# Performance work log

Hardware: AMD Instinct MI355X
Metric: run time of the kernel (lower is better)

The kernel has to match this reference:

```python
import jax, jax.numpy as jnp
import numpy as np

E = 192; Q = 48; H = 3; HD = Q // H  # per-branch embed 48, 3 heads of 16
CONV_CH = 4; K = 15; PAD = K // 2


def layer_norm(x, g, b, eps=1e-6):
    m = jnp.mean(x, axis=-1, keepdims=True)
    v = jnp.mean((x - m) ** 2, axis=-1, keepdims=True)
    return (x - m) * jax.lax.rsqrt(v + eps) * g + b


def mha(x, w_in, b_in, w_o, b_o):
    # x: [B,S,48]; torch nn.MultiheadAttention math (dropout=eval/identity)
    B, S, _ = x.shape
    qkv = x @ w_in.T + b_in                      # [B,S,144]
    q, k, v = jnp.split(qkv, 3, axis=-1)
    q = q.reshape(B, S, H, HD)
    k = k.reshape(B, S, H, HD)
    v = v.reshape(B, S, H, HD)
    scores = jnp.einsum('bqhd,bkhd->bhqk', q, k) / jnp.sqrt(jnp.float32(HD))
    attn = jax.nn.softmax(scores, axis=-1)
    out = jnp.einsum('bhqk,bkhd->bqhd', attn, v).reshape(B, S, Q)
    return out @ w_o.T + b_o


def light_conv(x96, conv_w):
    # x96: [B,S,96] -> view(-1, 4, 96), depthwise conv1d (k=15, pad=7), view back
    B, S, W = x96.shape
    r = x96.reshape(-1, CONV_CH, W)              # [B*S/... wait: B*S*96/(4*96)=B*S/4? No: reshape(-1,4,96) => [B*S, ...]
    y = jax.lax.conv_general_dilated(
        r, conv_w, window_strides=(1,), padding=[(PAD, PAD)],
        dimension_numbers=('NCH', 'OIH', 'NCH'), feature_group_count=CONV_CH)
    return y.reshape(B, S, W)


def setup_inputs() -> dict:
    key = jax.random.key(0)
    ks = jax.random.split(key, 16)
    sc = 0.05
    d = {
        'x': jax.random.normal(ks[0], (128, 512, E), dtype=jnp.float32),
        'ln1_g': jnp.ones((E,), jnp.float32), 'ln1_b': jnp.zeros((E,), jnp.float32),
        'acc_wqkv': jax.random.normal(ks[1], (3 * Q, Q), jnp.float32) * sc,
        'acc_bqkv': jnp.zeros((3 * Q,), jnp.float32),
        'acc_wo': jax.random.normal(ks[2], (Q, Q), jnp.float32) * sc,
        'acc_bo': jnp.zeros((Q,), jnp.float32),
        'gyro_wqkv': jax.random.normal(ks[3], (3 * Q, Q), jnp.float32) * sc,
        'gyro_bqkv': jnp.zeros((3 * Q,), jnp.float32),
        'gyro_wo': jax.random.normal(ks[4], (Q, Q), jnp.float32) * sc,
        'gyro_bo': jnp.zeros((Q,), jnp.float32),
        'conv_w': jax.random.normal(ks[5], (CONV_CH, 1, K), jnp.float32) * sc,
        'ln2_g': jnp.ones((E,), jnp.float32), 'ln2_b': jnp.zeros((E,), jnp.float32),
        'w1': jax.random.normal(ks[6], (2 * E, E), jnp.float32) * sc,
        'b1': jnp.zeros((2 * E,), jnp.float32),
        'w2': jax.random.normal(ks[7], (E, 2 * E), jnp.float32) * sc,
        'b2': jnp.zeros((E,), jnp.float32),
    }
    return d


def reference(x, ln1_g, ln1_b, acc_wqkv, acc_bqkv, acc_wo, acc_bo,
              gyro_wqkv, gyro_bqkv, gyro_wo, gyro_bo, conv_w,
              ln2_g, ln2_b, w1, b1, w2, b2):
    xn = layer_norm(x, ln1_g, ln1_b)
    x_conv = light_conv(xn[:, :, 48:144], conv_w)
    x_acc = mha(xn[:, :, 0:48], acc_wqkv, acc_bqkv, acc_wo, acc_bo)
    x_gyro = mha(xn[:, :, 96:144], gyro_wqkv, gyro_bqkv, gyro_wo, gyro_bo)
    xcat = jnp.concatenate([x_acc, x_conv, x_gyro], axis=2)
    x1 = xcat + x
    tt = layer_norm(x1, ln2_g, ln2_b)
    tt = jax.nn.relu(tt @ w1.T + b1)
    tt = jax.nn.relu(tt @ w2.T + b2)
    return x1 + tt
```

## Files before the change

kernel.cpp:

```cpp
#include <hip/hip_runtime.h>
#include <stdint.h>

typedef unsigned short u16;
typedef short bf16x8 __attribute__((ext_vector_type(8)));
typedef float f32x4 __attribute__((ext_vector_type(4)));
typedef float f32x16 __attribute__((ext_vector_type(16)));
typedef uint32_t u32x4 __attribute__((ext_vector_type(4)));

#define NB   128
#define SEQ  512
#define EMB  192
#define NTOK (NB * SEQ)
#define F1DIM 384
#define ATTW 192
#define VTP  520
#define KTS  24
#define XnS  200
#define H1S  392

__device__ __forceinline__ float bf2f(u16 u) {
  union { uint32_t u; float f; } v; v.u = ((uint32_t)u) << 16; return v.f;
}
__device__ __forceinline__ u16 f2bf(float f) {
  union { float f; uint32_t u; } v; v.f = f;
  uint32_t r = v.u + 0x7fffu + ((v.u >> 16) & 1u);
  return (u16)(r >> 16);
}
__device__ __forceinline__ uint32_t pack2bf(float a, float b) {
  return (uint32_t)f2bf(a) | ((uint32_t)f2bf(b) << 16);
}

__global__ __launch_bounds__(256) void pack_kernel(const float* __restrict__ w1,
    const float* __restrict__ w2, const float* __restrict__ wqa,
    const float* __restrict__ wqg, const float* __restrict__ woa,
    const float* __restrict__ wog, u16* __restrict__ w1b, u16* __restrict__ w2b,
    u16* __restrict__ wqp, u16* __restrict__ wop) {
  int idx = (int)blockIdx.x * 256 + (int)threadIdx.x;
  if (idx < 73728) {
    w1b[idx] = f2bf(w1[idx]);
  } else if (idx < 147456) {
    w2b[idx - 73728] = f2bf(w2[idx - 73728]);
  } else if (idx < 165888) {
    int i = idx - 147456;
    int row = i >> 6, k = i & 63;
    float v = 0.0f;
    if (k < 48) v = (row < 144) ? wqa[row * 48 + k] : wqg[(row - 144) * 48 + k];
    wqp[i] = f2bf(v);
  } else if (idx < 172032) {
    int i = idx - 165888;
    int row = i >> 6, k = i & 63;
    float v = 0.0f;
    if (k < 48) v = (row < 48) ? woa[row * 48 + k] : wog[(row - 48) * 48 + k];
    wop[i] = f2bf(v);
  }
}

__global__ __launch_bounds__(256) void ln1_qkv_conv_kernel(
    const float* __restrict__ x, const float* __restrict__ g,
    const float* __restrict__ b, const u16* __restrict__ wq,
    const float* __restrict__ bacc, const float* __restrict__ bgyr,
    const float* __restrict__ cw, u16* __restrict__ qkv,
    u16* __restrict__ att) {
  __shared__ u16 Xn[64 * XnS];
  int bm = (int)blockIdx.x * 64;
  int tid = threadIdx.x;
  int trow = tid >> 2, part = tid & 3;
  int tok = bm + trow;
  const float* xr = x + (size_t)tok * EMB + part * 48;
  float vals[48];
#pragma unroll
  for (int j = 0; j < 48; j += 4) {
    float4 v = *(const float4*)(xr + j);
    vals[j] = v.x; vals[j + 1] = v.y; vals[j + 2] = v.z; vals[j + 3] = v.w;
  }
  float s = 0.0f, s2 = 0.0f;
#pragma unroll
  for (int j = 0; j < 48; j++) { s += vals[j]; s2 += vals[j] * vals[j]; }
  s += __shfl_xor(s, 1); s2 += __shfl_xor(s2, 1);
  s += __shfl_xor(s, 2); s2 += __shfl_xor(s2, 2);
  float mean = s * (1.0f / EMB);
  float var  = s2 * (1.0f / EMB) - mean * mean;
  float rs   = rsqrtf(var + 1e-6f);
  {
    u16* xnrow = Xn + trow * XnS + part * 48;
    const float* gp = g + part * 48;
    const float* bp = b + part * 48;
#pragma unroll
    for (int j = 0; j < 48; j += 2) {
      uint32_t w = pack2bf((vals[j] - mean) * rs * gp[j] + bp[j],
                           (vals[j + 1] - mean) * rs * gp[j + 1] + bp[j + 1]);
      *(uint32_t*)(xnrow + j) = w;
    }
  }
  __syncthreads();
  int wid = tid >> 6, lane = tid & 63;
  int l15 = lane & 15, quad = lane >> 4;
  const u16* arow_l = Xn + (wid * 16 + l15) * XnS;
  f32x4 acc[18] = {};
#pragma unroll
  for (int ks = 0; ks < 2; ks++) {
    int kk = ks * 32;
    bf16x8 af_a = *(const bf16x8*)(arow_l + kk + quad * 8);
    bf16x8 af_g = *(const bf16x8*)(arow_l + 96 + kk + quad * 8);
#pragma unroll
    for (int st = 0; st < 18; st++) {
      bf16x8 bf = *(const bf16x8*)(wq + (size_t)(st * 16 + l15) * 64 + kk + quad * 8);
      acc[st] = __builtin_amdgcn_mfma_f32_16x16x32_bf16(st < 9 ? af_a : af_g,
                                                        bf, acc[st], 0, 0, 0);
    }
  }
#pragma unroll
  for (int st = 0; st < 18; st++) {
    int col = st * 16 + l15;
    int cc = (col < 144) ? col : col - 144;
    float bias = (col < 144) ? bacc[cc] : bgyr[cc];
    float qs = (cc < 48) ? 0.36067376022f : 1.0f;
#pragma unroll
    for (int r = 0; r < 4; r++) {
      int orow = bm + wid * 16 + quad * 4 + r;
      qkv[(size_t)orow * 288 + col] = f2bf((acc[st][r] + bias) * qs);
    }
  }
  {
    int wr = trow & 3;
    float w15[15];
#pragma unroll
    for (int k = 0; k < 15; k++) w15[k] = cw[wr * 15 + k];
    float win[38];
    int base = part * 24 - 7;
#pragma unroll
    for (int i = 0; i < 38; i++) {
      int p = base + i;
      win[i] = (p >= 0 && p < 96) ? bf2f(Xn[trow * XnS + 48 + p]) : 0.0f;
    }
    const float* xres = x + (size_t)tok * EMB + 48 + part * 24;
    u16* orow = att + (size_t)tok * ATTW + 96 + part * 24;
#pragma unroll
    for (int c = 0; c < 24; c += 4) {
      float4 r4 = *(const float4*)(xres + c);
      float o[4];
#pragma unroll
      for (int u = 0; u < 4; u++) {
        float sc = 0.0f;
#pragma unroll
        for (int k = 0; k < 15; k++) sc += win[c + u + k] * w15[k];
        o[u] = sc;
      }
      *(uint32_t*)(orow + c)     = pack2bf(o[0] + r4.x, o[1] + r4.y);
      *(uint32_t*)(orow + c + 2) = pack2bf(o[2] + r4.z, o[3] + r4.w);
    }
  }
}

__global__ __launch_bounds__(256) void attn_kernel(const u16* __restrict__ qkv,
                                                   u16* __restrict__ att) {
  __shared__ u16 Kt[SEQ * KTS];
  __shared__ u16 Vt[17 * VTP];
  int bid = blockIdx.x;
  int hh  = bid % 3;
  int brb = (bid / 3) & 1;
  int b   = bid / 6;
  int tid = threadIdx.x;
  size_t tokbase = (size_t)b * SEQ;
  int qoff = brb * 144 + hh * 16;
  int koff = qoff + 48;
  int voff = qoff + 96;
  for (int r = tid; r < SEQ; r += 256) {
    const u16* src = qkv + (tokbase + r) * 288;
    *(uint4*)(Kt + r * KTS)     = *(const uint4*)(src + koff);
    *(uint4*)(Kt + r * KTS + 8) = *(const uint4*)(src + koff + 8);
    u16 tmp[16];
    *(uint4*)(tmp)     = *(const uint4*)(src + voff);
    *(uint4*)(tmp + 8) = *(const uint4*)(src + voff + 8);
#pragma unroll
    for (int j = 0; j < 16; j++) Vt[j * VTP + r] = tmp[j];
  }
  Vt[16 * VTP + tid]       = 0x3F80;
  Vt[16 * VTP + 256 + tid] = 0x3F80;
  __syncthreads();
  int wave = tid >> 6, lane = tid & 63;
  int q31 = lane & 31, h = lane >> 5;
  int dcl = (q31 < 16) ? q31 : 16;
#pragma unroll 1
  for (int qi = 0; qi < 4; qi++) {
    int qrow = (wave * 4 + qi) * 32 + q31;
    bf16x8 qfrag = *(const bf16x8*)(qkv + (tokbase + qrow) * 288 + qoff + h * 8);
    f32x16 Ot = {};
#pragma unroll 2
    for (int kt = 0; kt < 16; kt++) {
      bf16x8 kfrag = *(const bf16x8*)(Kt + (kt * 32 + q31) * KTS + h * 8);
      f32x16 zc = {};
      f32x16 S = __builtin_amdgcn_mfma_f32_32x32x16_bf16(kfrag, qfrag, zc, 0, 0, 0);
      uint32_t pk[8], swk[8];
#pragma unroll
      for (int i = 0; i < 8; i++) {
        union { float f; uint32_t u; } a0, a1;
        a0.f = exp2f(S[2 * i]);
        a1.f = exp2f(S[2 * i + 1]);
        pk[i] = __builtin_amdgcn_perm(a1.u, a0.u, 0x07060302u);
        swk[i] = (uint32_t)__shfl_xor((int)pk[i], 32);
      }
      u32x4 t1 = { h ? swk[2] : pk[0], h ? swk[3] : pk[1],
                   h ? pk[2]  : swk[0], h ? pk[3]  : swk[1] };
      u32x4 t2 = { h ? swk[6] : pk[4], h ? swk[7] : pk[5],
                   h ? pk[6]  : swk[4], h ? pk[7]  : swk[5] };
      bf16x8 pb1 = __builtin_bit_cast(bf16x8, t1);
      bf16x8 pb2 = __builtin_bit_cast(bf16x8, t2);
      bf16x8 av1 = *(const bf16x8*)(Vt + dcl * VTP + kt * 32 + h * 8);
      bf16x8 av2 = *(const bf16x8*)(Vt + dcl * VTP + kt * 32 + 16 + h * 8);
      Ot = __builtin_amdgcn_mfma_f32_32x32x16_bf16(av1, pb1, Ot, 0, 0, 0);
      Ot = __builtin_amdgcn_mfma_f32_32x32x16_bf16(av2, pb2, Ot, 0, 0, 0);
    }
    float inv = 1.0f / Ot[8];
    u16* orow = att + (tokbase + qrow) * ATTW + brb * 48 + hh * 16 + 4 * h;
    uint2 st0 = { pack2bf(Ot[0] * inv, Ot[1] * inv),
                  pack2bf(Ot[2] * inv, Ot[3] * inv) };
    uint2 st1 = { pack2bf(Ot[4] * inv, Ot[5] * inv),
                  pack2bf(Ot[6] * inv, Ot[7] * inv) };
    *(uint2*)(orow)     = st0;
    *(uint2*)(orow + 8) = st1;
  }
}

__global__ __launch_bounds__(256) void tail_kernel(
    const u16* __restrict__ att, const u16* __restrict__ wo,
    const float* __restrict__ boacc, const float* __restrict__ bogyr,
    const float* __restrict__ x, const float* __restrict__ g2,
    const float* __restrict__ b2v, const u16* __restrict__ w1b,
    const float* __restrict__ b1, const u16* __restrict__ w2b,
    const float* __restrict__ b2, float* __restrict__ out) {
  __shared__ u16 LDSB[32 * XnS + 32 * H1S];
  u16* X1b = LDSB;
  u16* Tn  = LDSB + 32 * XnS;
  u16* H1  = LDSB + 32 * XnS;
  int bm = (int)blockIdx.x * 32;
  int tid = threadIdx.x;
  int wid = tid >> 6, lane = tid & 63;
  int l15 = lane & 15, quad = lane >> 4;
  {
    int trow = tid >> 3, p8 = tid & 7;
    const u16* src = att + (size_t)(bm + trow) * ATTW + 96 + p8 * 12;
    u16* dst = X1b + trow * XnS + 48 + p8 * 12;
    *(uint2*)(dst)     = *(const uint2*)(src);
    *(uint2*)(dst + 4) = *(const uint2*)(src + 4);
    *(uint2*)(dst + 8) = *(const uint2*)(src + 8);
  }
  {
    int mt = wid & 1, ng = wid >> 1;
    int row = bm + mt * 16 + l15;
    const u16* arow = att + (size_t)row * ATTW + (ng ? 48 : 0);
    f32x4 acc[3] = {};
#pragma unroll
    for (int ks = 0; ks < 2; ks++) {
      int kk = ks * 32;
      bf16x8 af = *(const bf16x8*)(arow + kk + quad * 8);
#pragma unroll
      for (int st = 0; st < 3; st++) {
        int stg = ng * 3 + st;
        bf16x8 bf = *(const bf16x8*)(wo + (size_t)(stg * 16 + l15) * 64 + kk + quad * 8);
        acc[st] = __builtin_amdgcn_mfma_f32_16x16x32_bf16(af, bf, acc[st], 0, 0, 0);
      }
    }
#pragma unroll
    for (int st = 0; st < 3; st++) {
      int col = (ng * 3 + st) * 16 + l15;
      float bias = (col < 48) ? boacc[col] : bogyr[col - 48];
      int oc = (col < 48) ? col : col + 96;
#pragma unroll
      for (int r = 0; r < 4; r++) {
        int lrow = mt * 16 + quad * 4 + r;
        float v = acc[st][r] + bias + x[(size_t)(bm + lrow) * EMB + oc];
        X1b[lrow * XnS + oc] = f2bf(v);
      }
    }
  }
  __syncthreads();
  {
    int trow = tid >> 3, part = tid & 7;
    const u16* xl = X1b + trow * XnS + part * 24;
    float vals[24];
    {
      u16 raw[24];
      *(uint4*)(raw)      = *(const uint4*)(xl);
      *(uint4*)(raw + 8)  = *(const uint4*)(xl + 8);
      *(uint4*)(raw + 16) = *(const uint4*)(xl + 16);
#pragma unroll
      for (int j = 0; j < 24; j++) vals[j] = bf2f(raw[j]);
    }
    float s = 0.0f, s2 = 0.0f;
#pragma unroll
    for (int j = 0; j < 24; j++) { s += vals[j]; s2 += vals[j] * vals[j]; }
    s += __shfl_xor(s, 1); s2 += __shfl_xor(s2, 1);
    s += __shfl_xor(s, 2); s2 += __shfl_xor(s2, 2);
    s += __shfl_xor(s, 4); s2 += __shfl_xor(s2, 4);
    float mean = s * (1.0f / EMB);
    float var  = s2 * (1.0f / EMB) - mean * mean;
    float rs   = rsqrtf(var + 1e-6f);
    u16* trp = Tn + trow * XnS + part * 24;
    const float* gp = g2 + part * 24;
    const float* bp = b2v + part * 24;
#pragma unroll
    for (int j = 0; j < 24; j += 2) {
      uint32_t w = pack2bf((vals[j] - mean) * rs * gp[j] + bp[j],
                           (vals[j + 1] - mean) * rs * gp[j + 1] + bp[j + 1]);
      *(uint32_t*)(trp + j) = w;
    }
  }
  __syncthreads();
  int ng1 = wid;
  f32x4 acc1[12] = {};
#pragma unroll
  for (int kk = 0; kk < 192; kk += 32) {
    bf16x8 a0 = *(const bf16x8*)(Tn + (l15) * XnS + kk + quad * 8);
    bf16x8 a1 = *(const bf16x8*)(Tn + (16 + l15) * XnS + kk + quad * 8);
#pragma unroll
    for (int stl = 0; stl < 6; stl++) {
      bf16x8 bf = *(const bf16x8*)(w1b + (size_t)((ng1 * 6 + stl) * 16 + l15) * EMB + kk + quad * 8);
      acc1[stl]     = __builtin_amdgcn_mfma_f32_16x16x32_bf16(a0, bf, acc1[stl], 0, 0, 0);
      acc1[6 + stl] = __builtin_amdgcn_mfma_f32_16x16x32_bf16(a1, bf, acc1[6 + stl], 0, 0, 0);
    }
  }
  __syncthreads();
#pragma unroll
  for (int stl = 0; stl < 6; stl++) {
    int col = (ng1 * 6 + stl) * 16 + l15;
    float bias = b1[col];
#pragma unroll
    for (int m2 = 0; m2 < 2; m2++) {
#pragma unroll
      for (int r = 0; r < 4; r++) {
        float v = acc1[m2 * 6 + stl][r] + bias;
        v = v > 0.0f ? v : 0.0f;
        H1[(m2 * 16 + quad * 4 + r) * H1S + col] = f2bf(v);
      }
    }
  }
  __syncthreads();
  {
    int ng2 = wid;
    f32x4 acc2[6] = {};
#pragma unroll
    for (int kk = 0; kk < 384; kk += 32) {
      bf16x8 a0 = *(const bf16x8*)(H1 + (l15) * H1S + kk + quad * 8);
      bf16x8 a1 = *(const bf16x8*)(H1 + (16 + l15) * H1S + kk + quad * 8);
#pragma unroll
      for (int stl = 0; stl < 3; stl++) {
        bf16x8 bf = *(const bf16x8*)(w2b + (size_t)((ng2 * 3 + stl) * 16 + l15) * F1DIM + kk + quad * 8);
        acc2[stl]     = __builtin_amdgcn_mfma_f32_16x16x32_bf16(a0, bf, acc2[stl], 0, 0, 0);
        acc2[3 + stl] = __builtin_amdgcn_mfma_f32_16x16x32_bf16(a1, bf, acc2[3 + stl], 0, 0, 0);
      }
    }
#pragma unroll
    for (int stl = 0; stl < 3; stl++) {
      int col = (ng2 * 3 + stl) * 16 + l15;
      float bias = b2[col];
#pragma unroll
      for (int m2 = 0; m2 < 2; m2++) {
#pragma unroll
        for (int r = 0; r < 4; r++) {
          int lrow = m2 * 16 + quad * 4 + r;
          float v = acc2[m2 * 3 + stl][r] + bias;
          v = v > 0.0f ? v : 0.0f;
          out[(size_t)(bm + lrow) * EMB + col] = v + bf2f(X1b[lrow * XnS + col]);
        }
      }
    }
  }
}

extern "C" void kernel_launch(void* const* d_in, const int* in_sizes, int n_in,
                              void* d_out, int out_size, void* d_ws, size_t ws_size,
                              hipStream_t stream) {
  const float* x         = (const float*)d_in[0];
  const float* ln1_g     = (const float*)d_in[1];
  const float* ln1_b     = (const float*)d_in[2];
  const float* acc_wqkv  = (const float*)d_in[3];
  const float* acc_bqkv  = (const float*)d_in[4];
  const float* acc_wo    = (const float*)d_in[5];
  const float* acc_bo    = (const float*)d_in[6];
  const float* gyro_wqkv = (const float*)d_in[7];
  const float* gyro_bqkv = (const float*)d_in[8];
  const float* gyro_wo   = (const float*)d_in[9];
  const float* gyro_bo   = (const float*)d_in[10];
  const float* conv_w    = (const float*)d_in[11];
  const float* ln2_g     = (const float*)d_in[12];
  const float* ln2_b     = (const float*)d_in[13];
  const float* w1        = (const float*)d_in[14];
  const float* b1        = (const float*)d_in[15];
  const float* w2        = (const float*)d_in[16];
  const float* b2        = (const float*)d_in[17];
  float* out = (float*)d_out;
  char* ws = (char*)d_ws;

  u16* qkvb = (u16*)(ws);
  u16* attb = (u16*)(ws + 37748736);
  u16* w1b  = (u16*)(ws + 62914560);
  u16* w2b  = (u16*)(ws + 63062016);
  u16* wqp  = (u16*)(ws + 63209472);
  u16* wop  = (u16*)(ws + 63246336);

  pack_kernel<<<672, 256, 0, stream>>>(w1, w2, acc_wqkv, gyro_wqkv, acc_wo,
                                       gyro_wo, w1b, w2b, wqp, wop);
  ln1_qkv_conv_kernel<<<NTOK / 64, 256, 0, stream>>>(
      x, ln1_g, ln1_b, wqp, acc_bqkv, gyro_bqkv, conv_w, qkvb, attb);
  attn_kernel<<<NB * 6, 256, 0, stream>>>(qkvb, attb);
  tail_kernel<<<NTOK / 32, 256, 0, stream>>>(
      attb, wop, acc_bo, gyro_bo, x, ln2_g, ln2_b, w1b, b1, w2b, b2, out);
}
```

Baseline: 317.6 us.

## Halve tail kernel row tile to 16 and prefetch first MLP weight fragments

The tail kernel now processes 16 tokens per block instead of 32, which halves the accumulator registers and LDS per block and doubles the grid, with a launch bound asking for 6 blocks per CU. The first k-slice of the W1 and W2 fragments is loaded into registers at kernel start so those loads overlap the out-projection and layernorm phases. The out-projection work is redistributed: three waves do the MFMAs and one wave copies the conv columns. In exchange, each weight fragment is reused across only one 16-row tile, so global/L2 weight traffic per token doubles.

Result: slower. 395.4 us (+24.5%).

```diff
diff --git a/kernel.cpp b/kernel.cpp
--- a/kernel.cpp
+++ b/kernel.cpp
@@ -222,147 +222,161 @@
   }
 }
 
-__global__ __launch_bounds__(256) void tail_kernel(
+__global__ __launch_bounds__(256, 6) void tail_kernel(
     const u16* __restrict__ att, const u16* __restrict__ wo,
     const float* __restrict__ boacc, const float* __restrict__ bogyr,
     const float* __restrict__ x, const float* __restrict__ g2,
     const float* __restrict__ b2v, const u16* __restrict__ w1b,
     const float* __restrict__ b1, const u16* __restrict__ w2b,
     const float* __restrict__ b2, float* __restrict__ out) {
-  __shared__ u16 LDSB[32 * XnS + 32 * H1S];
+  __shared__ u16 LDSB[32 * XnS + 16 * H1S];
   u16* X1b = LDSB;
-  u16* Tn  = LDSB + 32 * XnS;
+  u16* Tn  = LDSB + 16 * XnS;
   u16* H1  = LDSB + 32 * XnS;
-  int bm = (int)blockIdx.x * 32;
+  int bm = (int)blockIdx.x * 16;
   int tid = threadIdx.x;
   int wid = tid >> 6, lane = tid & 63;
   int l15 = lane & 15, quad = lane >> 4;
-  {
-    int trow = tid >> 3, p8 = tid & 7;
-    const u16* src = att + (size_t)(bm + trow) * ATTW + 96 + p8 * 12;
-    u16* dst = X1b + trow * XnS + 48 + p8 * 12;
-    *(uint2*)(dst)     = *(const uint2*)(src);
-    *(uint2*)(dst + 4) = *(const uint2*)(src + 4);
-    *(uint2*)(dst + 8) = *(const uint2*)(src + 8);
-  }
-  {
-    int mt = wid & 1, ng = wid >> 1;
-    int row = bm + mt * 16 + l15;
-    const u16* arow = att + (size_t)row * ATTW + (ng ? 48 : 0);
-    f32x4 acc[3] = {};
+
+  bf16x8 pw1[6], pw2[3];
+#pragma unroll
+  for (int stl = 0; stl < 6; stl++)
+    pw1[stl] = *(const bf16x8*)(w1b + (size_t)((wid * 6 + stl) * 16 + l15) * EMB + quad * 8);
+#pragma unroll
+  for (int stl = 0; stl < 3; stl++)
+    pw2[stl] = *(const bf16x8*)(w2b + (size_t)((wid * 3 + stl) * 16 + l15) * F1DIM + quad * 8);
+
+  if (wid == 3) {
+    int trow = lane >> 2, p4 = lane & 3;
+    const u16* src = att + (size_t)(bm + trow) * ATTW + 96 + p4 * 24;
+    u16* dst = X1b + trow * XnS + 48 + p4 * 24;
+    *(uint4*)(dst)      = *(const uint4*)(src);
+    *(uint4*)(dst + 8)  = *(const uint4*)(src + 8);
+    *(uint4*)(dst + 16) = *(const uint4*)(src + 16);
+  } else {
+    const u16* arow0 = att + (size_t)(bm + l15) * ATTW;
+    bf16x8 afA[2], afG[2];
 #pragma unroll
     for (int ks = 0; ks < 2; ks++) {
-      int kk = ks * 32;
-      bf16x8 af = *(const bf16x8*)(arow + kk + quad * 8);
-#pragma unroll
-      for (int st = 0; st < 3; st++) {
-        int stg = ng * 3 + st;
-        bf16x8 bf = *(const bf16x8*)(wo + (size_t)(stg * 16 + l15) * 64 + kk + quad * 8);
-        acc[st] = __builtin_amdgcn_mfma_f32_16x16x32_bf16(af, bf, acc[st], 0, 0, 0);
-      }
-    }
-#pragma unroll
-    for (int st = 0; st < 3; st++) {
-      int col = (ng * 3 + st) * 16 + l15;
+      afA[ks] = *(const bf16x8*)(arow0 + ks * 32 + quad * 8);
+      afG[ks] = *(const bf16x8*)(arow0 + 48 + ks * 32 + quad * 8);
+    }
+    f32x4 acc[2] = {};
+#pragma unroll
+    for (int s = 0; s < 2; s++) {
+      int st = wid * 2 + s;
+      int ng = (st >= 3) ? 1 : 0;
+#pragma unroll
+      for (int ks = 0; ks < 2; ks++) {
+        bf16x8 bf = *(const bf16x8*)(wo + (size_t)(st * 16 + l15) * 64 + ks * 32 + quad * 8);
+        acc[s] = __builtin_amdgcn_mfma_f32_16x16x32_bf16(ng ? afG[ks] : afA[ks],
+                                                         bf, acc[s], 0, 0, 0);
+      }
+    }
+#pragma unroll
+    for (int s = 0; s < 2; s++) {
+      int st = wid * 2 + s;
+      int col = st * 16 + l15;
       float bias = (col < 48) ? boacc[col] : bogyr[col - 48];
       int oc = (col < 48) ? col : col + 96;
 #pragma unroll
       for (int r = 0; r < 4; r++) {
-        int lrow = mt * 16 + quad * 4 + r;
-        float v = acc[st][r] + bias + x[(size_t)(bm + lrow) * EMB + oc];
+        int lrow = quad * 4 + r;
+        float v = acc[s][r] + bias + x[(size_t)(bm + lrow) * EMB + oc];
         X1b[lrow * XnS + oc] = f2bf(v);
       }
     }
   }
   __syncthreads();
+
   {
-    int trow = tid >> 3, part = tid & 7;
-    const u16* xl = X1b + trow * XnS + part * 24;
-    float vals[24];
-    {
-      u16 raw[24];
-      *(uint4*)(raw)      = *(const uint4*)(xl);
-      *(uint4*)(raw + 8)  = *(const uint4*)(xl + 8);
-      *(uint4*)(raw + 16) = *(const uint4*)(xl + 16);
-#pragma unroll
-      for (int j = 0; j < 24; j++) vals[j] = bf2f(raw[j]);
-    }
+    int trow = tid >> 4, part = tid & 15;
+    const u16* xl = X1b + trow * XnS + part * 12;
+    u16 raw[12];
+    *(uint2*)(raw)     = *(const uint2*)(xl);
+    *(uint2*)(raw + 4) = *(const uint2*)(xl + 4);
+    *(uint2*)(raw + 8) = *(const uint2*)(xl + 8);
+    float vals[12];
+#pragma unroll
+    for (int j = 0; j < 12; j++) vals[j] = bf2f(raw[j]);
     float s = 0.0f, s2 = 0.0f;
 #pragma unroll
-    for (int j = 0; j < 24; j++) { s += vals[j]; s2 += vals[j] * vals[j]; }
+    for (int j = 0; j < 12; j++) { s += vals[j]; s2 += vals[j] * vals[j]; }
     s += __shfl_xor(s, 1); s2 += __shfl_xor(s2, 1);
     s += __shfl_xor(s, 2); s2 += __shfl_xor(s2, 2);
     s += __shfl_xor(s, 4); s2 += __shfl_xor(s2, 4);
+    s += __shfl_xor(s, 8); s2 += __shfl_xor(s2, 8);
     float mean = s * (1.0f / EMB);
     float var  = s2 * (1.0f / EMB) - mean * mean;
     float rs   = rsqrtf(var + 1e-6f);
-    u16* trp = Tn + trow * XnS + part * 24;
-    const float* gp = g2 + part * 24;
-    const float* bp = b2v + part * 24;
-#pragma unroll
-    for (int j = 0; j < 24; j += 2) {
+    u16* trp = Tn + trow * XnS + part * 12;
+    const float* gp = g2 + part * 12;
+    const float* bp = b2v + part * 12;
+#pragma unroll
+    for (int j = 0; j < 12; j += 2) {
       uint32_t w = pack2bf((vals[j] - mean) * rs * gp[j] + bp[j],
                            (vals[j + 1] - mean) * rs * gp[j + 1] + bp[j + 1]);
       *(uint32_t*)(trp + j) = w;
     }
   }
   __syncthreads();
-  int ng1 = wid;
-  f32x4 acc1[12] = {};
-#pragma unroll
-  for (int kk = 0; kk < 192; kk += 32) {
-    bf16x8 a0 = *(const bf16x8*)(Tn + (l15) * XnS + kk + quad * 8);
-    bf16x8 a1 = *(const bf16x8*)(Tn + (16 + l15) * XnS + kk + quad * 8);
+
+  f32x4 acc1[6] = {};
+  {
+    bf16x8 a0 = *(const bf16x8*)(Tn + l15 * XnS + quad * 8);
+#pragma unroll
+    for (int stl = 0; stl < 6; stl++)
+      acc1[stl] = __builtin_amdgcn_mfma_f32_16x16x32_bf16(a0, pw1[stl], acc1[stl], 0, 0, 0);
+  }
+#pragma unroll
+  for (int kk = 32; kk < 192; kk += 32) {
+    bf16x8 a0 = *(const bf16x8*)(Tn + l15 * XnS + kk + quad * 8);
 #pragma unroll
     for (int stl = 0; stl < 6; stl++) {
-      bf16x8 bf = *(const bf16x8*)(w1b + (size_t)((ng1 * 6 + stl) * 16 + l15) * EMB + kk + quad * 8);
-      acc1[stl]     = __builtin_amdgcn_mfma_f32_16x16x32_bf16(a0, bf, acc1[stl], 0, 0, 0);
-      acc1[6 + stl] = __builtin_amdgcn_mfma_f32_16x16x32_bf16(a1, bf, acc1[6 + stl], 0, 0, 0);
+      bf16x8 bf = *(const bf16x8*)(w1b + (size_t)((wid * 6 + stl) * 16 + l15) * EMB + kk + quad * 8);
+      acc1[stl] = __builtin_amdgcn_mfma_f32_16x16x32_bf16(a0, bf, acc1[stl], 0, 0, 0);
+    }
+  }
+#pragma unroll
+  for (int stl = 0; stl < 6; stl++) {
+    int col = (wid * 6 + stl) * 16 + l15;
+    float bias = b1[col];
+#pragma unroll
+    for (int r = 0; r < 4; r++) {
+      float v = acc1[stl][r] + bias;
+      v = v > 0.0f ? v : 0.0f;
+      H1[(quad * 4 + r) * H1S + col] = f2bf(v);
     }
   }
   __syncthreads();
-#pragma unroll
-  for (int stl = 0; stl < 6; stl++) {
-    int col = (ng1 * 6 + stl) * 16 + l15;
-    float bias = b1[col];
-#pragma unroll
-    for (int m2 = 0; m2 < 2; m2++) {
+
+  {
+    f32x4 acc2[3] = {};
+    {
+      bf16x8 a0 = *(const bf16x8*)(H1 + l15 * H1S + quad * 8);
+#pragma unroll
+      for (int stl = 0; stl < 3; stl++)
+        acc2[stl] = __builtin_amdgcn_mfma_f32_16x16x32_bf16(a0, pw2[stl], acc2[stl], 0, 0, 0);
+    }
+#pragma unroll
+    for (int kk = 32; kk < 384; kk += 32) {
+      bf16x8 a0 = *(const bf16x8*)(H1 + l15 * H1S + kk + quad * 8);
+#pragma unroll
+      for (int stl = 0; stl < 3; stl++) {
+        bf16x8 bf = *(const bf16x8*)(w2b + (size_t)((wid * 3 + stl) * 16 + l15) * F1DIM + kk + quad * 8);
+        acc2[stl] = __builtin_amdgcn_mfma_f32_16x16x32_bf16(a0, bf, acc2[stl], 0, 0, 0);
+      }
+    }
+#pragma unroll
+    for (int stl = 0; stl < 3; stl++) {
+      int col = (wid * 3 + stl) * 16 + l15;
+      float bias = b2[col];
 #pragma unroll
       for (int r = 0; r < 4; r++) {
-        float v = acc1[m2 * 6 + stl][r] + bias;
+        int lrow = quad * 4 + r;
+        float v = acc2[stl][r] + bias;
         v = v > 0.0f ? v : 0.0f;
-        H1[(m2 * 16 + quad * 4 + r) * H1S + col] = f2bf(v);
-      }
-    }
-  }
-  __syncthreads();
-  {
-    int ng2 = wid;
-    f32x4 acc2[6] = {};
-#pragma unroll
-    for (int kk = 0; kk < 384; kk += 32) {
-      bf16x8 a0 = *(const bf16x8*)(H1 + (l15) * H1S + kk + quad * 8);
-      bf16x8 a1 = *(const bf16x8*)(H1 + (16 + l15) * H1S + kk + quad * 8);
-#pragma unroll
-      for (int stl = 0; stl < 3; stl++) {
-        bf16x8 bf = *(const bf16x8*)(w2b + (size_t)((ng2 * 3 + stl) * 16 + l15) * F1DIM + kk + quad * 8);
-        acc2[stl]     = __builtin_amdgcn_mfma_f32_16x16x32_bf16(a0, bf, acc2[stl], 0, 0, 0);
-        acc2[3 + stl] = __builtin_amdgcn_mfma_f32_16x16x32_bf16(a1, bf, acc2[3 + stl], 0, 0, 0);
-      }
-    }
-#pragma unroll
-    for (int stl = 0; stl < 3; stl++) {
-      int col = (ng2 * 3 + stl) * 16 + l15;
-      float bias = b2[col];
-#pragma unroll
-      for (int m2 = 0; m2 < 2; m2++) {
-#pragma unroll
-        for (int r = 0; r < 4; r++) {
-          int lrow = m2 * 16 + quad * 4 + r;
-          float v = acc2[m2 * 3 + stl][r] + bias;
-          v = v > 0.0f ? v : 0.0f;
-          out[(size_t)(bm + lrow) * EMB + col] = v + bf2f(X1b[lrow * XnS + col]);
-        }
+        out[(size_t)(bm + lrow) * EMB + col] = v + bf2f(X1b[lrow * XnS + col]);
       }
     }
   }
@@ -404,6 +418,6 @@
   ln1_qkv_conv_kernel<<<NTOK / 64, 256, 0, stream>>>(
       x, ln1_g, ln1_b, wqp, acc_bqkv, gyro_bqkv, conv_w, qkvb, attb);
   attn_kernel<<<NB * 6, 256, 0, stream>>>(qkvb, attb);
-  tail_kernel<<<NTOK / 32, 256, 0, stream>>>(
+  tail_kernel<<<NTOK / 16, 256, 0, stream>>>(
       attb, wop, acc_bo, gyro_bo, x, ln2_g, ln2_b, w1b, b1, w2b, b2, out);
 }
```
